# Performance work log

Measured on AMD Instinct MI355X. Metric: run time of the kernel, lower is better.

The kernel has to match this reference:

```python
import jax, jax.numpy as jnp
import numpy as np

N_TOKEN = 267735
CUTS = [0, 20000, 40000, 200000, 267735]
DIV = 4
D_MODEL = 1024
N_HEAD = 16
D_HEAD = 64
D_INNER = 4096
N_LAYER = 4
QLEN = 512
MLEN = 512
BSZ = 4
EPS = 1e-5


def _ln(x, g, b):
    mu = jnp.mean(x, axis=-1, keepdims=True)
    var = jnp.var(x, axis=-1, keepdims=True)
    return (x - mu) * jax.lax.rsqrt(var + EPS) * g + b


def _rel_shift(x):
    # x: [qlen, klen, bsz, n_head]
    q, k, b, n = x.shape
    x = jnp.pad(x, ((0, 0), (1, 0), (0, 0), (0, 0)))
    x = x.reshape(k + 1, q, b, n)[1:]
    return x.reshape(q, k, b, n)


def setup_inputs() -> dict:
    key = jax.random.key(0)
    ks = list(jax.random.split(key, 32))
    p = lambda i, shape: 0.02 * jax.random.normal(ks[i], shape, dtype=jnp.float32)
    inp = {}
    inp['input_ids'] = jax.random.randint(ks[0], (BSZ, QLEN), 0, N_TOKEN, dtype=jnp.int32)
    inp['mems'] = 0.05 * jax.random.normal(ks[1], (N_LAYER, MLEN, BSZ, D_MODEL), dtype=jnp.float32)
    # adaptive embedding: cluster tables + projections (div_val=4)
    for i in range(4):
        l, r = CUTS[i], CUTS[i + 1]
        d_i = D_MODEL // (DIV ** i)
        inp[f'emb{i}'] = p(2 + i, (r - l, d_i))
        inp[f'proj{i}'] = p(6 + i, (d_i, D_MODEL))
    H = N_HEAD * D_HEAD
    inp['qkv_W'] = p(10, (N_LAYER, D_MODEL, 3 * H))
    inp['r_W'] = p(11, (N_LAYER, D_MODEL, H))
    inp['o_W'] = p(12, (N_LAYER, H, D_MODEL))
    inp['r_w_bias'] = p(13, (N_LAYER, N_HEAD, D_HEAD))
    inp['r_r_bias'] = p(14, (N_LAYER, N_HEAD, D_HEAD))
    inp['ln1_g'] = jnp.ones((N_LAYER, D_MODEL), jnp.float32)
    inp['ln1_b'] = jnp.zeros((N_LAYER, D_MODEL), jnp.float32)
    inp['ff_w1'] = p(15, (N_LAYER, D_MODEL, D_INNER))
    inp['ff_b1'] = jnp.zeros((N_LAYER, D_INNER), jnp.float32)
    inp['ff_w2'] = p(16, (N_LAYER, D_INNER, D_MODEL))
    inp['ff_b2'] = jnp.zeros((N_LAYER, D_MODEL), jnp.float32)
    inp['ln2_g'] = jnp.ones((N_LAYER, D_MODEL), jnp.float32)
    inp['ln2_b'] = jnp.zeros((N_LAYER, D_MODEL), jnp.float32)
    return inp


def _forward(input_ids, mems, embs, projs, qkv_W, r_W, o_W, r_w_bias, r_r_bias,
             ln1_g, ln1_b, ff_w1, ff_b1, ff_w2, ff_b2, ln2_g, ln2_b):
    ids = input_ids.T  # [qlen, bsz]
    qlen, bsz = ids.shape
    mems = jax.lax.stop_gradient(mems)  # mems are detached in the original
    mlen = mems.shape[1]
    klen = qlen + mlen

    # --- adaptive embedding (masked gather + scatter-add, same math as boolean_mask/scatter_nd) ---
    flat = ids.reshape(-1)
    emb = jnp.zeros((flat.shape[0], D_MODEL), jnp.float32)
    for i in range(4):
        l, r = CUTS[i], CUTS[i + 1]
        mask = (flat >= l) & (flat < r)
        idx = jnp.clip(flat - l, 0, r - l - 1)
        e_i = jnp.einsum('id,de->ie', embs[i][idx], projs[i])
        emb = emb + jnp.where(mask[:, None], e_i, 0.0)
    word_emb = (emb * (D_MODEL ** 0.5)).reshape(qlen, bsz, D_MODEL)

    # --- sinusoidal relative positions, pos_seq = klen-1 .. 0 ---
    pos_seq = jnp.arange(klen - 1, -1, -1, dtype=jnp.float32)
    inv_freq = 1.0 / (10000.0 ** (jnp.arange(0, D_MODEL, 2, dtype=jnp.float32) / D_MODEL))
    sinusoid = jnp.einsum('i,j->ij', pos_seq, inv_freq)
    pos_emb = jnp.concatenate([jnp.sin(sinusoid), jnp.cos(sinusoid)], axis=-1)  # [klen, d_model]

    # causal mask over memory-extended keys: [qlen, klen]
    attn_mask = jnp.triu(jnp.ones((qlen, klen), jnp.float32), k=1 + mlen)
    mask4 = attn_mask[:, :, None, None]
    scale = 1.0 / (D_HEAD ** 0.5)

    h = word_emb
    for l in range(N_LAYER):
        cat = jnp.concatenate([mems[l], h], axis=0)  # [klen, bsz, d_model]
        w_heads = jnp.einsum('kbd,dh->kbh', cat, qkv_W[l])
        r_head_k = jnp.einsum('kd,dh->kh', pos_emb, r_W[l]).reshape(klen, N_HEAD, D_HEAD)
        q_h, k_h, v_h = jnp.split(w_heads, 3, axis=-1)
        q_h = q_h[-qlen:].reshape(qlen, bsz, N_HEAD, D_HEAD)
        k_h = k_h.reshape(klen, bsz, N_HEAD, D_HEAD)
        v_h = v_h.reshape(klen, bsz, N_HEAD, D_HEAD)
        AC = jnp.einsum('ibnd,jbnd->ijbn', q_h + r_w_bias[l], k_h)
        BD = _rel_shift(jnp.einsum('ibnd,jnd->ijbn', q_h + r_r_bias[l], r_head_k))
        score = (AC + BD) * scale
        score = score * (1.0 - mask4) - 1e30 * mask4
        prob = jax.nn.softmax(score, axis=1)
        attn_vec = jnp.einsum('ijbn,jbnd->ibnd', prob, v_h).reshape(qlen, bsz, N_HEAD * D_HEAD)
        attn_out = jnp.einsum('ibh,hd->ibd', attn_vec, o_W[l])
        h = _ln(h + attn_out, ln1_g[l], ln1_b[l])
        ff = jnp.einsum('ibf,fd->ibd', jax.nn.relu(jnp.einsum('ibd,df->ibf', h, ff_w1[l]) + ff_b1[l]), ff_w2[l]) + ff_b2[l]
        h = _ln(h + ff, ln2_g[l], ln2_b[l])

    return h.transpose(1, 0, 2)  # [bsz, qlen, d_model]


def reference(input_ids, mems, emb0, emb1, emb2, emb3, proj0, proj1, proj2, proj3,
              qkv_W, r_W, o_W, r_w_bias, r_r_bias, ln1_g, ln1_b,
              ff_w1, ff_b1, ff_w2, ff_b2, ln2_g, ln2_b):
    return _forward(input_ids, mems, (emb0, emb1, emb2, emb3), (proj0, proj1, proj2, proj3),
                    qkv_W, r_W, o_W, r_w_bias, r_r_bias, ln1_g, ln1_b,
                    ff_w1, ff_b1, ff_w2, ff_b2, ln2_g, ln2_b)
```

## Files before the change

### kernel.cpp

```cpp
#include <hip/hip_runtime.h>

typedef __attribute__((ext_vector_type(8))) short bf16x8;
typedef __attribute__((ext_vector_type(4))) float f32x4;

#define N_LAYER 4
#define QLEN 512
#define MLEN 512
#define KLEN 1024
#define BSZ 4
#define DM 1024
#define NH 16
#define DH 64
#define DINNER 4096
#define EK 1408
#define BDLD 1152

__device__ __forceinline__ unsigned short f2bf(float x) {
    unsigned u = __float_as_uint(x);
    u += 0x7fffu + ((u >> 16) & 1u);
    return (unsigned short)(u >> 16);
}
__device__ __forceinline__ float bf2f(unsigned short v) {
    return __uint_as_float(((unsigned)v) << 16);
}

__device__ __forceinline__ void gload16(const unsigned short* g, unsigned short* l) {
    __builtin_amdgcn_global_load_lds(
        (const __attribute__((address_space(1))) unsigned int*)g,
        (__attribute__((address_space(3))) unsigned int*)l, 16, 0, 0);
}

__device__ __forceinline__ bf16x8 lds_read8_sw(const unsigned short* base, int row, int cb) {
    return *(const bf16x8*)((const char*)base + row * 128 + (cb ^ ((row & 7) << 4)));
}

__global__ __launch_bounds__(256)
void transpose_all(const float* __restrict__ qkvWl, const float* __restrict__ rWl,
                   const float* __restrict__ oWl, const float* __restrict__ w1l,
                   const float* __restrict__ w2l,
                   unsigned short* __restrict__ qkvT, unsigned short* __restrict__ rT,
                   unsigned short* __restrict__ oT, unsigned short* __restrict__ w1T,
                   unsigned short* __restrict__ w2T) {
    __shared__ float tile[64][65];
    int id = blockIdx.x;
    const float* W; unsigned short* D; int K, N, bx, by;
    if (id < 768)       { W = qkvWl; D = qkvT; K = 1024; N = 3072; bx = id % 48; by = id / 48; }
    else if (id < 1024) { id -= 768;  W = rWl;  D = rT;  K = 1024; N = 1024; bx = id & 15; by = id >> 4; }
    else if (id < 1280) { id -= 1024; W = oWl;  D = oT;  K = 1024; N = 1024; bx = id & 15; by = id >> 4; }
    else if (id < 2304) { id -= 1280; W = w1l;  D = w1T; K = 1024; N = 4096; bx = id & 63; by = id >> 6; }
    else                { id -= 2304; W = w2l;  D = w2T; K = 4096; N = 1024; bx = id & 15; by = id >> 4; }
    const int tid = threadIdx.x;
#pragma unroll
    for (int s = 0; s < 4; ++s) {
        int idx = s * 256 + tid;
        int kr = idx >> 4, c4 = (idx & 15) * 4;
        float4 v = *(const float4*)(W + (size_t)(by * 64 + kr) * N + bx * 64 + c4);
        tile[kr][c4] = v.x; tile[kr][c4 + 1] = v.y;
        tile[kr][c4 + 2] = v.z; tile[kr][c4 + 3] = v.w;
    }
    __syncthreads();
#pragma unroll
    for (int s = 0; s < 2; ++s) {
        int idx = s * 256 + tid;
        int nl = idx >> 3, k8 = (idx & 7) * 8;
        unsigned short tmp[8];
#pragma unroll
        for (int j = 0; j < 8; ++j) tmp[j] = f2bf(tile[k8 + j][nl]);
        *(uint4*)(D + (size_t)(bx * 64 + nl) * K + by * 64 + k8) = *(uint4*)tmp;
    }
}

__global__ __launch_bounds__(256)
void transpose_pad(const float* __restrict__ W, unsigned short* __restrict__ dst,
                   int K, int N, int dstLD, int dstOff) {
    __shared__ float tile[32][33];
    const int tx = threadIdx.x & 31, ty = threadIdx.x >> 5;
    const int bx = blockIdx.x, by = blockIdx.y;
#pragma unroll
    for (int i = 0; i < 4; ++i) {
        int k = by * 32 + ty + i * 8;
        tile[ty + i * 8][tx] = (k < K) ? W[(size_t)k * N + bx * 32 + tx] : 0.f;
    }
    __syncthreads();
#pragma unroll
    for (int i = 0; i < 4; ++i) {
        int n = bx * 32 + ty + i * 8;
        int k = by * 32 + tx;
        dst[(size_t)n * dstLD + dstOff + k] = f2bf(tile[tx][ty + i * 8]);
    }
}

__global__ __launch_bounds__(256)
void emb_gather(const int* __restrict__ ids,
                const float* __restrict__ e0, const float* __restrict__ e1,
                const float* __restrict__ e2, const float* __restrict__ e3,
                unsigned short* __restrict__ embA) {
    const int chunk = blockIdx.x * 256 + threadIdx.x;
    if (chunk >= 2048 * 176) return;
    const int t = chunk / 176;
    const int e8 = (chunk - t * 176) * 8;
    const int i = t >> 2, b = t & 3;
    const int id = ids[b * QLEN + i];
    const float* src = nullptr;
    if (e8 < 1024) {
        if (id < 20000) src = e0 + (size_t)id * 1024 + e8;
    } else if (e8 < 1280) {
        if (id >= 20000 && id < 40000) src = e1 + (size_t)(id - 20000) * 256 + (e8 - 1024);
    } else if (e8 < 1344) {
        if (id >= 40000 && id < 200000) src = e2 + (size_t)(id - 40000) * 64 + (e8 - 1280);
    } else if (e8 < 1360) {
        if (id >= 200000) src = e3 + (size_t)(id - 200000) * 16 + (e8 - 1344);
    }
    uint4 o = {0u, 0u, 0u, 0u};
    if (src) {
        float4 v0 = *(const float4*)src;
        float4 v1 = *(const float4*)(src + 4);
        o.x = (unsigned)f2bf(v0.x * 32.f) | ((unsigned)f2bf(v0.y * 32.f) << 16);
        o.y = (unsigned)f2bf(v0.z * 32.f) | ((unsigned)f2bf(v0.w * 32.f) << 16);
        o.z = (unsigned)f2bf(v1.x * 32.f) | ((unsigned)f2bf(v1.y * 32.f) << 16);
        o.w = (unsigned)f2bf(v1.z * 32.f) | ((unsigned)f2bf(v1.w * 32.f) << 16);
    }
    *(uint4*)(embA + (size_t)t * EK + e8) = o;
}

template <int MODE, int BN>
__global__ __launch_bounds__(256)
void gemm_bt(const unsigned short* __restrict__ A, const unsigned short* __restrict__ BT,
             float* __restrict__ C, unsigned short* __restrict__ Cbf,
             const float* __restrict__ bias,
             const float* __restrict__ rwb, const float* __restrict__ rrb,
             unsigned short* __restrict__ Qw, unsigned short* __restrict__ Qr,
             unsigned short* __restrict__ Kb, unsigned short* __restrict__ VTb,
             int M, int N, int K) {
    constexpr int NF = BN / 32;
    __shared__ unsigned short lA[2][128 * 64];
    __shared__ unsigned short lB[2][BN * 64];
    const int tid = threadIdx.x;
    const int w = tid >> 6, l = tid & 63;
    const int lane15 = l & 15, lh = l >> 4;
    const int nwg = gridDim.x;
    const int cpx = nwg >> 3;
    const int swz = (blockIdx.x & 7) * cpx + (blockIdx.x >> 3);
    const int nbn = N / BN;
    const int bm = swz / nbn, bn = swz % nbn;
    const int wr = (w >> 1) * 64, wc = (w & 1) * (BN / 2);

    f32x4 acc[4][NF] = {};

    const unsigned short* gA = A + (size_t)(bm * 128) * K;
    const unsigned short* gB = BT + (size_t)(bn * BN) * K;

    auto stage = [&](int buf, int k0) {
#pragma unroll
        for (int s = 0; s < 4; ++s) {
            int g = tid + s * 256, row = g >> 3;
            gload16(gA + (size_t)row * K + k0 + ((g & 7) ^ (row & 7)) * 8,
                    lA[buf] + g * 8);
        }
#pragma unroll
        for (int s = 0; s < BN / 32; ++s) {
            int g = tid + s * 256, row = g >> 3;
            gload16(gB + (size_t)row * K + k0 + ((g & 7) ^ (row & 7)) * 8,
                    lB[buf] + g * 8);
        }
    };

    stage(0, 0);
    __syncthreads();
    int cur = 0;
    for (int k0 = 0; k0 < K; k0 += 64) {
        if (k0 + 64 < K) stage(cur ^ 1, k0 + 64);
        const unsigned short* cA = lA[cur];
        const unsigned short* cB = lB[cur];
#pragma unroll
        for (int kk = 0; kk < 2; ++kk) {
            bf16x8 af[4], bfr[NF];
#pragma unroll
            for (int f = 0; f < 4; ++f)
                af[f] = lds_read8_sw(cA, wr + f * 16 + lane15, kk * 64 + lh * 16);
#pragma unroll
            for (int f = 0; f < NF; ++f)
                bfr[f] = lds_read8_sw(cB, wc + f * 16 + lane15, kk * 64 + lh * 16);
#pragma unroll
            for (int mi = 0; mi < 4; ++mi)
#pragma unroll
                for (int ni = 0; ni < NF; ++ni)
                    acc[mi][ni] = __builtin_amdgcn_mfma_f32_16x16x32_bf16(
                        af[mi], bfr[ni], acc[mi][ni], 0, 0, 0);
        }
        __syncthreads();
        cur ^= 1;
    }

#pragma unroll
    for (int mi = 0; mi < 4; ++mi) {
        int rowb = bm * 128 + wr + mi * 16 + lh * 4;
#pragma unroll
        for (int ni = 0; ni < NF; ++ni) {
            int col = bn * BN + wc + ni * 16 + lane15;
#pragma unroll
            for (int r = 0; r < 4; ++r) {
                float x = acc[mi][ni][r];
                if (MODE == 0) {
                    C[(size_t)(rowb + r) * N + col] = x;
                } else if (MODE == 1) {
                    x += bias[col];
                    Cbf[(size_t)(rowb + r) * N + col] = f2bf(x > 0.f ? x : 0.f);
                } else if (MODE == 2) {
                    C[(size_t)(rowb + r) * N + col] = x + bias[col];
                } else if (MODE == 3) {
                    int j = rowb >> 2;
                    int bb_ = r;
                    if (col < 1024) {
                        if (j >= MLEN) {
                            int i = j - MLEN, n = col >> 6, d = col & 63;
                            size_t o = ((size_t)(bb_ * NH + n) * QLEN + i) * DH + d;
                            Qw[o] = f2bf((x + rwb[col]) * 0.125f);
                            Qr[o] = f2bf(x + rrb[col]);
                        }
                    } else if (col < 2048) {
                        int c2 = col - 1024, n = c2 >> 6, d = c2 & 63;
                        Kb[((size_t)(bb_ * NH + n) * KLEN + j) * DH + d] = f2bf(x);
                    } else {
                        int c2 = col - 2048, n = c2 >> 6, d = c2 & 63;
                        VTb[((size_t)(bb_ * NH + n) * DH + d) * KLEN + j] = f2bf(x);
                    }
                } else {
                    int j = rowb + r;
                    int n = col >> 6, d = col & 63;
                    Kb[((size_t)n * KLEN + j) * DH + d] = f2bf(x);
                }
            }
        }
    }
}

__global__ __launch_bounds__(256)
void bd_gemm(const unsigned short* __restrict__ Qr, const unsigned short* __restrict__ Rb,
             unsigned short* __restrict__ BDs) {
    __shared__ unsigned short lA[128 * 64];
    __shared__ unsigned short lB[128 * 64];
    const int tid = threadIdx.x;
    const int w = tid >> 6, l = tid & 63;
    const int lane15 = l & 15, lh = l >> 4;
    const int blk = blockIdx.x;
    const int bn = blk & 63;
    const int tile = blk >> 6;
    const int mi_ = tile & 3, nj = tile >> 2;
    const int n = bn & 15;
    const int wr = (w >> 1) * 64, wc = (w & 1) * 64;

    const unsigned short* gA = Qr + (size_t)bn * QLEN * DH + (size_t)(mi_ * 128) * 64;
    const unsigned short* gB = Rb + (size_t)n * KLEN * DH + (size_t)(nj * 128) * 64;
#pragma unroll
    for (int s = 0; s < 4; ++s) {
        int g = tid + s * 256, row = g >> 3;
        gload16(gA + (size_t)row * 64 + ((g & 7) ^ (row & 7)) * 8, lA + g * 8);
        gload16(gB + (size_t)row * 64 + ((g & 7) ^ (row & 7)) * 8, lB + g * 8);
    }
    __syncthreads();
    f32x4 acc[4][4] = {};
#pragma unroll
    for (int kk = 0; kk < 2; ++kk) {
        bf16x8 af[4], bfr[4];
#pragma unroll
        for (int f = 0; f < 4; ++f) {
            af[f]  = lds_read8_sw(lA, wr + f * 16 + lane15, kk * 64 + lh * 16);
            bfr[f] = lds_read8_sw(lB, wc + f * 16 + lane15, kk * 64 + lh * 16);
        }
#pragma unroll
        for (int mi = 0; mi < 4; ++mi)
#pragma unroll
            for (int ni = 0; ni < 4; ++ni)
                acc[mi][ni] = __builtin_amdgcn_mfma_f32_16x16x32_bf16(
                    af[mi], bfr[ni], acc[mi][ni], 0, 0, 0);
    }
    unsigned short* out = BDs + (size_t)bn * 512 * BDLD;
#pragma unroll
    for (int mi = 0; mi < 4; ++mi) {
        int rowb = mi_ * 128 + wr + mi * 16 + lh * 4;
#pragma unroll
        for (int ni = 0; ni < 4; ++ni) {
            int col = nj * 128 + wc + ni * 16 + lane15;
#pragma unroll
            for (int r = 0; r < 4; ++r)
                out[(size_t)(rowb + r) * BDLD + col] = f2bf(acc[mi][ni][r] * 0.125f);
        }
    }
}

__global__ __launch_bounds__(256)
void pos_kernel(unsigned short* __restrict__ posbf) {
    const int p = blockIdx.x, tid = threadIdx.x;
    const float ps = (float)(KLEN - 1 - p);
    const float c = -2.0f * 9.210340371976184f / 1024.0f;
#pragma unroll
    for (int j4 = 0; j4 < 4; ++j4) {
        int j = tid + j4 * 256;
        int m = (j < 512) ? j : j - 512;
        float freq = __expf((float)m * c);
        float ang = ps * freq;
        float v = (j < 512) ? sinf(ang) : cosf(ang);
        posbf[(size_t)p * DM + j] = f2bf(v);
    }
}

__global__ __launch_bounds__(256)
void cat_kernel(const float* __restrict__ mem_l, const float* __restrict__ h,
                unsigned short* __restrict__ catbf) {
    const int t = blockIdx.x, tid = threadIdx.x;
    const float* src = (t < 2048) ? (mem_l + (size_t)t * DM) : (h + (size_t)(t - 2048) * DM);
    float4 v = ((const float4*)src)[tid];
    uint2 o;
    o.x = (unsigned)f2bf(v.x) | ((unsigned)f2bf(v.y) << 16);
    o.y = (unsigned)f2bf(v.z) | ((unsigned)f2bf(v.w) << 16);
    ((uint2*)(catbf + (size_t)t * DM))[tid] = o;
}

__global__ __launch_bounds__(64)
void attn_part(const unsigned short* __restrict__ Qw,
               const unsigned short* __restrict__ Kb, const unsigned short* __restrict__ VTb,
               const unsigned short* __restrict__ BDs,
               unsigned short* __restrict__ Opart, float* __restrict__ ms) {
    __shared__ unsigned short lP[16 * 64];

    const int l = threadIdx.x;
    const int lane15 = l & 15, lh = l >> 4;
    const int blk = blockIdx.x;
    const int bn = blk & 63;
    const int rest = blk >> 6;
    const int rg = rest & 3;
    const int c = rest >> 2;

    const int offt[8] = {0, 3, 7, 11, 15, 20, 25, 30};
    const int nctt[8] = {3, 4, 4, 4, 5, 5, 5, 6};
    int it = 0;
#pragma unroll
    for (int i = 1; i < 8; ++i) if (c >= offt[i]) it = i;
    const int cl = c - offt[it];
    const int nck = nctt[it];
    const int ntiles = it + 9;
    const int jt0 = (cl * ntiles) / nck;
    const int jt1 = ((cl + 1) * ntiles) / nck;
    const int i0 = it * 64;
    const int rowl = rg * 16 + lh * 4;

    bf16x8 qw[2];
    {
        size_t qb = ((size_t)bn * QLEN + i0 + rg * 16 + lane15) * DH + lh * 8;
        qw[0] = *(const bf16x8*)(Qw + qb);
        qw[1] = *(const bf16x8*)(Qw + qb + 32);
    }
    bf16x8 onesb;
#pragma unroll
    for (int j = 0; j < 8; ++j) onesb[j] = (short)0x3F80;

    const unsigned short* kp = Kb + (size_t)bn * KLEN * DH + (size_t)(jt0 * 64 + lane15) * DH + lh * 8;
    const unsigned short* vp = VTb + (size_t)bn * DH * KLEN + (size_t)lane15 * KLEN + jt0 * 64 + lh * 8;
    const unsigned short* bdp[4];
#pragma unroll
    for (int r = 0; r < 4; ++r) {
        int row = i0 + rowl + r;
        bdp[r] = BDs + (size_t)bn * 512 * BDLD + (size_t)row * BDLD
                 + (511 - row) + jt0 * 64 + lane15;
    }

    f32x4 oacc[4] = {};
    f32x4 srowv = {};

    for (int jt = jt0; jt < jt1; ++jt) {
        float bdv[4][4];
#pragma unroll
        for (int f = 0; f < 4; ++f)
#pragma unroll
            for (int r = 0; r < 4; ++r)
                bdv[f][r] = bf2f(bdp[r][16 * f]);

        bf16x8 kf[2][4];
#pragma unroll
        for (int f = 0; f < 4; ++f) {
            const unsigned short* p = kp + (size_t)(f * 16) * DH;
            kf[0][f] = *(const bf16x8*)p;
            kf[1][f] = *(const bf16x8*)(p + 32);
        }

        f32x4 sac[4] = {};
        __builtin_amdgcn_s_setprio(1);
#pragma unroll
        for (int kk = 0; kk < 2; ++kk)
#pragma unroll
            for (int f = 0; f < 4; ++f)
                sac[f] = __builtin_amdgcn_mfma_f32_16x16x32_bf16(qw[kk], kf[kk][f], sac[f], 0, 0, 0);
        __builtin_amdgcn_s_setprio(0);

        bf16x8 vf[2][4];
#pragma unroll
        for (int kk = 0; kk < 2; ++kk)
#pragma unroll
            for (int f = 0; f < 4; ++f)
                vf[kk][f] = *(const bf16x8*)(vp + (size_t)(f * 16) * KLEN + kk * 32);

        const bool lastTile = (jt == it + 8);
        float pv[4][4];
#pragma unroll
        for (int f = 0; f < 4; ++f) {
            int lj = lane15 + 16 * f;
#pragma unroll
            for (int r = 0; r < 4; ++r) {
                float s = sac[f][r] + bdv[f][r];
                if (lastTile && (lj > rowl + r)) s = -1e30f;
                pv[f][r] = __expf(s - 8.f);
            }
        }

#pragma unroll
        for (int f = 0; f < 4; ++f)
#pragma unroll
            for (int r = 0; r < 4; ++r) {
                int row = lh * 4 + r, cb2 = (lane15 + 16 * f) * 2;
                *(unsigned short*)((char*)lP + row * 128 + (cb2 ^ ((row & 7) << 4))) =
                    f2bf(pv[f][r]);
            }
        bf16x8 pa[2];
        pa[0] = lds_read8_sw(lP, lane15, lh * 16);
        pa[1] = lds_read8_sw(lP, lane15, 64 + lh * 16);

        __builtin_amdgcn_s_setprio(1);
#pragma unroll
        for (int kk = 0; kk < 2; ++kk) {
#pragma unroll
            for (int f = 0; f < 4; ++f)
                oacc[f] = __builtin_amdgcn_mfma_f32_16x16x32_bf16(pa[kk], vf[kk][f], oacc[f], 0, 0, 0);
            srowv = __builtin_amdgcn_mfma_f32_16x16x32_bf16(pa[kk], onesb, srowv, 0, 0, 0);
        }
        __builtin_amdgcn_s_setprio(0);

        kp += 64 * DH;
        vp += 64;
#pragma unroll
        for (int r = 0; r < 4; ++r) bdp[r] += 64;
    }

    const int slot = (bn * 8 + it) * 6 + cl;
    unsigned short* Op = Opart + (size_t)slot * 4096;
#pragma unroll
    for (int f = 0; f < 4; ++f)
#pragma unroll
        for (int r = 0; r < 4; ++r)
            Op[(rowl + r) * 64 + lane15 + 16 * f] = f2bf(oacc[f][r]);
    if (lane15 == 0) {
        float* msp = ms + (size_t)slot * 64;
#pragma unroll
        for (int r = 0; r < 4; ++r) msp[rowl + r] = srowv[r];
    }
}

__global__ __launch_bounds__(256)
void attn_merge(const unsigned short* __restrict__ Opart, const float* __restrict__ ms,
                unsigned short* __restrict__ avec) {
    const int blk = blockIdx.x;
    const int bn = blk & 63, it = blk >> 6;
    const int n = bn & 15, b = bn >> 4;
    const int nctt[8] = {3, 4, 4, 4, 5, 5, 5, 6};
    const int k = nctt[it];
    const int tid = threadIdx.x;
    const int r = tid >> 2, cq = (tid & 3) * 16;
    const int base_slot = (bn * 8 + it) * 6;

    float S = 0.f;
    for (int c = 0; c < k; ++c) S += ms[(size_t)(base_slot + c) * 64 + r];

    float acc[16];
#pragma unroll
    for (int j = 0; j < 16; ++j) acc[j] = 0.f;
    for (int c = 0; c < k; ++c) {
        const bf16x8* op = (const bf16x8*)(Opart + (size_t)(base_slot + c) * 4096 + r * 64 + cq);
        bf16x8 v0 = op[0], v1 = op[1];
#pragma unroll
        for (int j = 0; j < 8; ++j) {
            acc[j]     += bf2f((unsigned short)v0[j]);
            acc[8 + j] += bf2f((unsigned short)v1[j]);
        }
    }
    float inv = 1.0f / S;
    int t = (it * 64 + r) * 4 + b;
    unsigned short* dst = avec + (size_t)t * DM + n * 64 + cq;
#pragma unroll
    for (int j = 0; j < 16; ++j) dst[j] = f2bf(acc[j] * inv);
}

__global__ __launch_bounds__(256)
void ln_kernel(const float* __restrict__ hin, const float* __restrict__ res,
               const float* __restrict__ g, const float* __restrict__ bb,
               float* __restrict__ hout, unsigned short* __restrict__ hbf) {
    __shared__ float ls[8];
    const int t = blockIdx.x, tid = threadIdx.x;
    float4 x = ((const float4*)(hin + (size_t)t * DM))[tid];
    float4 rr = ((const float4*)(res + (size_t)t * DM))[tid];
    float v0 = x.x + rr.x, v1 = x.y + rr.y, v2 = x.z + rr.z, v3 = x.w + rr.w;
    float s = v0 + v1 + v2 + v3;
    float sq = v0 * v0 + v1 * v1 + v2 * v2 + v3 * v3;
#pragma unroll
    for (int off = 1; off < 64; off <<= 1) {
        s += __shfl_xor(s, off);
        sq += __shfl_xor(sq, off);
    }
    const int w = tid >> 6;
    if ((tid & 63) == 0) { ls[w] = s; ls[4 + w] = sq; }
    __syncthreads();
    s = ls[0] + ls[1] + ls[2] + ls[3];
    sq = ls[4] + ls[5] + ls[6] + ls[7];
    float mu = s * (1.f / 1024.f);
    float var = sq * (1.f / 1024.f) - mu * mu;
    float rstd = rsqrtf(var + 1e-5f);
    float y[4] = {v0, v1, v2, v3};
    float4 of;
    uint2 ob;
    float* op = &of.x;
#pragma unroll
    for (int j = 0; j < 4; ++j) {
        int d = tid * 4 + j;
        op[j] = (y[j] - mu) * rstd * g[d] + bb[d];
    }
    ob.x = (unsigned)f2bf(of.x) | ((unsigned)f2bf(of.y) << 16);
    ob.y = (unsigned)f2bf(of.z) | ((unsigned)f2bf(of.w) << 16);
    ((float4*)(hout + (size_t)t * DM))[tid] = of;
    ((uint2*)(hbf + (size_t)t * DM))[tid] = ob;
}

__global__ __launch_bounds__(256)
void out_kernel(const float* __restrict__ h, float* __restrict__ out) {
    const int t = blockIdx.x, tid = threadIdx.x;
    const int i = t >> 2, b = t & 3;
    ((float4*)(out + ((size_t)b * QLEN + i) * DM))[tid] =
        ((const float4*)(h + (size_t)t * DM))[tid];
}

extern "C" void kernel_launch(void* const* d_in, const int* in_sizes, int n_in,
                              void* d_out, int out_size, void* d_ws, size_t ws_size,
                              hipStream_t stream) {
    const int* ids = (const int*)d_in[0];
    const float* mems = (const float*)d_in[1];
    const float* embp[4] = {nullptr, nullptr, nullptr, nullptr};
    const float* projp[4] = {nullptr, nullptr, nullptr, nullptr};
    const long long esz[4] = {20000LL * 1024, 20000LL * 256, 160000LL * 64, 67735LL * 16};
    const long long psz[4] = {1024LL * 1024, 256LL * 1024, 64LL * 1024, 16LL * 1024};
    for (int idx = 2; idx <= 9 && idx < n_in; ++idx) {
        long long s = in_sizes[idx];
        for (int c = 0; c < 4; ++c) {
            if (s == esz[c]) embp[c] = (const float*)d_in[idx];
            else if (s == psz[c]) projp[c] = (const float*)d_in[idx];
        }
    }
    const float* qkvW = (const float*)d_in[10];
    const float* rW   = (const float*)d_in[11];
    const float* oW   = (const float*)d_in[12];
    const float* rwb  = (const float*)d_in[13];
    const float* rrb  = (const float*)d_in[14];
    const float* ln1g = (const float*)d_in[15];
    const float* ln1b = (const float*)d_in[16];
    const float* ffw1 = (const float*)d_in[17];
    const float* ffb1 = (const float*)d_in[18];
    const float* ffw2 = (const float*)d_in[19];
    const float* ffb2 = (const float*)d_in[20];
    const float* ln2g = (const float*)d_in[21];
    const float* ln2b = (const float*)d_in[22];

    size_t off = 0;
    char* base = (char*)d_ws;
    auto alloc = [&](size_t bytes) -> char* {
        char* p = base + off;
        off = (off + bytes + 255) & ~(size_t)255;
        return p;
    };
    unsigned short* qkvT  = (unsigned short*)alloc(3072ull * 1024 * 2);
    unsigned short* rT    = (unsigned short*)alloc(1024ull * 1024 * 2);
    unsigned short* oT    = (unsigned short*)alloc(1024ull * 1024 * 2);
    unsigned short* w1T   = (unsigned short*)alloc(4096ull * 1024 * 2);
    unsigned short* w2T   = (unsigned short*)alloc(1024ull * 4096 * 2);
    unsigned short* embA  = (unsigned short*)alloc(2048ull * EK * 2);
    unsigned short* embBT = (unsigned short*)alloc(1024ull * EK * 2);
    float* h              = (float*)alloc(2048ull * 1024 * 4);
    unsigned short* hbf   = (unsigned short*)alloc(2048ull * 1024 * 2);
    unsigned short* catb  = (unsigned short*)alloc(4096ull * 1024 * 2);
    unsigned short* posb  = (unsigned short*)alloc(1024ull * 1024 * 2);
    unsigned short* Qw    = (unsigned short*)alloc(4ull * 16 * 512 * 64 * 2);
    unsigned short* Qr    = (unsigned short*)alloc(4ull * 16 * 512 * 64 * 2);
    unsigned short* Kb    = (unsigned short*)alloc(4ull * 16 * 1024 * 64 * 2);
    unsigned short* VTb   = (unsigned short*)alloc(4ull * 16 * 1024 * 64 * 2);
    unsigned short* Rb    = (unsigned short*)alloc(16ull * 1024 * 64 * 2);
    unsigned short* avec  = (unsigned short*)alloc(2048ull * 1024 * 2);
    float* resid          = (float*)alloc(2048ull * 1024 * 4);
    unsigned short* ff1b  = (unsigned short*)alloc(2048ull * 4096 * 2);
    unsigned short* Opart = (unsigned short*)alloc(3072ull * 4096 * 2);
    float* msbuf          = (float*)alloc(3072ull * 64 * 4);
    unsigned short* BDs   = (unsigned short*)alloc(64ull * 512 * BDLD * 2);
    (void)ws_size; (void)out_size;

    emb_gather<<<(2048 * 176 + 255) / 256, 256, 0, stream>>>(
        ids, embp[0], embp[1], embp[2], embp[3], embA);
    transpose_pad<<<dim3(32, 32), 256, 0, stream>>>(projp[0], embBT, 1024, 1024, EK, 0);
    transpose_pad<<<dim3(32, 8),  256, 0, stream>>>(projp[1], embBT, 256,  1024, EK, 1024);
    transpose_pad<<<dim3(32, 2),  256, 0, stream>>>(projp[2], embBT, 64,   1024, EK, 1280);
    transpose_pad<<<dim3(32, 2),  256, 0, stream>>>(projp[3], embBT, 16,   1024, EK, 1344);
    pos_kernel<<<1024, 256, 0, stream>>>(posb);
    gemm_bt<0, 128><<<(2048 / 128) * (1024 / 128), 256, 0, stream>>>(
        embA, embBT, h, nullptr, nullptr, nullptr, nullptr, nullptr, nullptr, nullptr, nullptr,
        2048, 1024, EK);

    for (int l = 0; l < N_LAYER; ++l) {
        const float* qkvWl = qkvW + (size_t)l * 1024 * 3072;
        const float* rWl   = rW + (size_t)l * 1024 * 1024;
        const float* oWl   = oW + (size_t)l * 1024 * 1024;
        const float* w1l   = ffw1 + (size_t)l * 1024 * 4096;
        const float* w2l   = ffw2 + (size_t)l * 4096 * 1024;

        transpose_all<<<3328, 256, 0, stream>>>(qkvWl, rWl, oWl, w1l, w2l,
                                                qkvT, rT, oT, w1T, w2T);

        cat_kernel<<<4096, 256, 0, stream>>>(mems + (size_t)l * 2048 * 1024, h, catb);

        gemm_bt<3, 128><<<(4096 / 128) * (3072 / 128), 256, 0, stream>>>(
            catb, qkvT, nullptr, nullptr, nullptr,
            rwb + l * 1024, rrb + l * 1024, Qw, Qr, Kb, VTb, 4096, 3072, 1024);

        gemm_bt<4, 64><<<(1024 / 128) * (1024 / 64), 256, 0, stream>>>(
            posb, rT, nullptr, nullptr, nullptr,
            nullptr, nullptr, nullptr, nullptr, Rb, nullptr, 1024, 1024, 1024);

        bd_gemm<<<64 * 32, 256, 0, stream>>>(Qr, Rb, BDs);

        attn_part<<<64 * 144, 64, 0, stream>>>(Qw, Kb, VTb, BDs, Opart, msbuf);
        attn_merge<<<512, 256, 0, stream>>>(Opart, msbuf, avec);

        gemm_bt<0, 64><<<(2048 / 128) * (1024 / 64), 256, 0, stream>>>(
            avec, oT, resid, nullptr, nullptr, nullptr, nullptr, nullptr, nullptr, nullptr, nullptr,
            2048, 1024, 1024);
        ln_kernel<<<2048, 256, 0, stream>>>(h, resid, ln1g + l * 1024, ln1b + l * 1024, h, hbf);

        gemm_bt<1, 128><<<(2048 / 128) * (4096 / 128), 256, 0, stream>>>(
            hbf, w1T, nullptr, ff1b, ffb1 + l * 4096, nullptr, nullptr, nullptr, nullptr, nullptr, nullptr,
            2048, 4096, 1024);
        gemm_bt<2, 64><<<(2048 / 128) * (1024 / 64), 256, 0, stream>>>(
            ff1b, w2T, resid, nullptr, ffb2 + l * 1024, nullptr, nullptr, nullptr, nullptr, nullptr, nullptr,
            2048, 1024, 4096);
        ln_kernel<<<2048, 256, 0, stream>>>(h, resid, ln2g + l * 1024, ln2b + l * 1024, h, hbf);
    }

    out_kernel<<<2048, 256, 0, stream>>>(h, (float*)d_out);
}
```

Measured before the change: 1.128 ms.

## Prefetch K/V tiles in attention and write h bf16 directly into concat buffer

```diff
diff --git a/kernel.cpp b/kernel.cpp
--- a/kernel.cpp
+++ b/kernel.cpp
@@ -225,10 +225,13 @@
                         int c2 = col - 2048, n = c2 >> 6, d = c2 & 63;
                         VTb[((size_t)(bb_ * NH + n) * DH + d) * KLEN + j] = f2bf(x);
                     }
-                } else {
+                } else if (MODE == 4) {
                     int j = rowb + r;
                     int n = col >> 6, d = col & 63;
                     Kb[((size_t)n * KLEN + j) * DH + d] = f2bf(x);
+                } else {
+                    C[(size_t)(rowb + r) * N + col] = x;
+                    Cbf[(size_t)(rowb + r) * N + col] = f2bf(x);
                 }
             }
         }
@@ -306,11 +309,9 @@
 }
 
 __global__ __launch_bounds__(256)
-void cat_kernel(const float* __restrict__ mem_l, const float* __restrict__ h,
-                unsigned short* __restrict__ catbf) {
+void mems_cat(const float* __restrict__ mem_l, unsigned short* __restrict__ catbf) {
     const int t = blockIdx.x, tid = threadIdx.x;
-    const float* src = (t < 2048) ? (mem_l + (size_t)t * DM) : (h + (size_t)(t - 2048) * DM);
-    float4 v = ((const float4*)src)[tid];
+    float4 v = ((const float4*)(mem_l + (size_t)t * DM))[tid];
     uint2 o;
     o.x = (unsigned)f2bf(v.x) | ((unsigned)f2bf(v.y) << 16);
     o.y = (unsigned)f2bf(v.z) | ((unsigned)f2bf(v.w) << 16);
@@ -342,6 +343,7 @@
     const int ntiles = it + 9;
     const int jt0 = (cl * ntiles) / nck;
     const int jt1 = ((cl + 1) * ntiles) / nck;
+    const int nt = jt1 - jt0;
     const int i0 = it * 64;
     const int rowl = rg * 16 + lh * 4;
 
@@ -368,21 +370,28 @@
     f32x4 oacc[4] = {};
     f32x4 srowv = {};
 
-    for (int jt = jt0; jt < jt1; ++jt) {
-        float bdv[4][4];
-#pragma unroll
-        for (int f = 0; f < 4; ++f)
-#pragma unroll
-            for (int r = 0; r < 4; ++r)
-                bdv[f][r] = bf2f(bdp[r][16 * f]);
-
-        bf16x8 kf[2][4];
+    auto loadt = [&](bf16x8 (&kf)[2][4], bf16x8 (&vf)[2][4], int d) {
 #pragma unroll
         for (int f = 0; f < 4; ++f) {
-            const unsigned short* p = kp + (size_t)(f * 16) * DH;
+            const unsigned short* p = kp + (size_t)(d * 64 + f * 16) * DH;
             kf[0][f] = *(const bf16x8*)p;
             kf[1][f] = *(const bf16x8*)(p + 32);
         }
+#pragma unroll
+        for (int kk = 0; kk < 2; ++kk)
+#pragma unroll
+            for (int f = 0; f < 4; ++f)
+                vf[kk][f] = *(const bf16x8*)(vp + d * 64 + (size_t)(f * 16) * KLEN + kk * 32);
+    };
+
+    auto computet = [&](bf16x8 (&kf)[2][4], bf16x8 (&vf)[2][4], int jt) {
+        const int d = jt - jt0;
+        float bdv[4][4];
+#pragma unroll
+        for (int f = 0; f < 4; ++f)
+#pragma unroll
+            for (int r = 0; r < 4; ++r)
+                bdv[f][r] = bf2f(bdp[r][d * 64 + 16 * f]);
 
         f32x4 sac[4] = {};
         __builtin_amdgcn_s_setprio(1);
@@ -392,13 +401,6 @@
             for (int f = 0; f < 4; ++f)
                 sac[f] = __builtin_amdgcn_mfma_f32_16x16x32_bf16(qw[kk], kf[kk][f], sac[f], 0, 0, 0);
         __builtin_amdgcn_s_setprio(0);
-
-        bf16x8 vf[2][4];
-#pragma unroll
-        for (int kk = 0; kk < 2; ++kk)
-#pragma unroll
-            for (int f = 0; f < 4; ++f)
-                vf[kk][f] = *(const bf16x8*)(vp + (size_t)(f * 16) * KLEN + kk * 32);
 
         const bool lastTile = (jt == it + 8);
         float pv[4][4];
@@ -412,7 +414,6 @@
                 pv[f][r] = __expf(s - 8.f);
             }
         }
-
 #pragma unroll
         for (int f = 0; f < 4; ++f)
 #pragma unroll
@@ -421,24 +422,31 @@
                 *(unsigned short*)((char*)lP + row * 128 + (cb2 ^ ((row & 7) << 4))) =
                     f2bf(pv[f][r]);
             }
-        bf16x8 pa[2];
-        pa[0] = lds_read8_sw(lP, lane15, lh * 16);
-        pa[1] = lds_read8_sw(lP, lane15, 64 + lh * 16);
+        bf16x8 pa0 = lds_read8_sw(lP, lane15, lh * 16);
+        bf16x8 pa1 = lds_read8_sw(lP, lane15, 64 + lh * 16);
 
         __builtin_amdgcn_s_setprio(1);
 #pragma unroll
-        for (int kk = 0; kk < 2; ++kk) {
-#pragma unroll
-            for (int f = 0; f < 4; ++f)
-                oacc[f] = __builtin_amdgcn_mfma_f32_16x16x32_bf16(pa[kk], vf[kk][f], oacc[f], 0, 0, 0);
-            srowv = __builtin_amdgcn_mfma_f32_16x16x32_bf16(pa[kk], onesb, srowv, 0, 0, 0);
-        }
+        for (int f = 0; f < 4; ++f)
+            oacc[f] = __builtin_amdgcn_mfma_f32_16x16x32_bf16(pa0, vf[0][f], oacc[f], 0, 0, 0);
+        srowv = __builtin_amdgcn_mfma_f32_16x16x32_bf16(pa0, onesb, srowv, 0, 0, 0);
+#pragma unroll
+        for (int f = 0; f < 4; ++f)
+            oacc[f] = __builtin_amdgcn_mfma_f32_16x16x32_bf16(pa1, vf[1][f], oacc[f], 0, 0, 0);
+        srowv = __builtin_amdgcn_mfma_f32_16x16x32_bf16(pa1, onesb, srowv, 0, 0, 0);
         __builtin_amdgcn_s_setprio(0);
-
-        kp += 64 * DH;
-        vp += 64;
-#pragma unroll
-        for (int r = 0; r < 4; ++r) bdp[r] += 64;
+    };
+
+    bf16x8 kfA[2][4], vfA[2][4], kfB[2][4], vfB[2][4];
+    loadt(kfA, vfA, 0);
+    if (nt >= 2) loadt(kfB, vfB, 1);
+    computet(kfA, vfA, jt0);
+    if (nt == 2) {
+        computet(kfB, vfB, jt0 + 1);
+    } else if (nt >= 3) {
+        loadt(kfA, vfA, 2);
+        computet(kfB, vfB, jt0 + 1);
+        computet(kfA, vfA, jt0 + 2);
     }
 
     const int slot = (bn * 8 + it) * 6 + cl;
@@ -597,6 +605,8 @@
     unsigned short* BDs   = (unsigned short*)alloc(64ull * 512 * BDLD * 2);
     (void)ws_size; (void)out_size;
 
+    unsigned short* catbHi = catb + 2048ull * 1024;
+
     emb_gather<<<(2048 * 176 + 255) / 256, 256, 0, stream>>>(
         ids, embp[0], embp[1], embp[2], embp[3], embA);
     transpose_pad<<<dim3(32, 32), 256, 0, stream>>>(projp[0], embBT, 1024, 1024, EK, 0);
@@ -604,8 +614,8 @@
     transpose_pad<<<dim3(32, 2),  256, 0, stream>>>(projp[2], embBT, 64,   1024, EK, 1280);
     transpose_pad<<<dim3(32, 2),  256, 0, stream>>>(projp[3], embBT, 16,   1024, EK, 1344);
     pos_kernel<<<1024, 256, 0, stream>>>(posb);
-    gemm_bt<0, 128><<<(2048 / 128) * (1024 / 128), 256, 0, stream>>>(
-        embA, embBT, h, nullptr, nullptr, nullptr, nullptr, nullptr, nullptr, nullptr, nullptr,
+    gemm_bt<5, 128><<<(2048 / 128) * (1024 / 128), 256, 0, stream>>>(
+        embA, embBT, h, catbHi, nullptr, nullptr, nullptr, nullptr, nullptr, nullptr, nullptr,
         2048, 1024, EK);
 
     for (int l = 0; l < N_LAYER; ++l) {
@@ -618,7 +628,7 @@
         transpose_all<<<3328, 256, 0, stream>>>(qkvWl, rWl, oWl, w1l, w2l,
                                                 qkvT, rT, oT, w1T, w2T);
 
-        cat_kernel<<<4096, 256, 0, stream>>>(mems + (size_t)l * 2048 * 1024, h, catb);
+        mems_cat<<<2048, 256, 0, stream>>>(mems + (size_t)l * 2048 * 1024, catb);
 
         gemm_bt<3, 128><<<(4096 / 128) * (3072 / 128), 256, 0, stream>>>(
             catb, qkvT, nullptr, nullptr, nullptr,
@@ -644,7 +654,8 @@
         gemm_bt<2, 64><<<(2048 / 128) * (1024 / 64), 256, 0, stream>>>(
             ff1b, w2T, resid, nullptr, ffb2 + l * 1024, nullptr, nullptr, nullptr, nullptr, nullptr, nullptr,
             2048, 1024, 4096);
-        ln_kernel<<<2048, 256, 0, stream>>>(h, resid, ln2g + l * 1024, ln2b + l * 1024, h, hbf);
+        ln_kernel<<<2048, 256, 0, stream>>>(h, resid, ln2g + l * 1024, ln2b + l * 1024, h,
+                                            (l < 3) ? catbHi : hbf);
     }
 
     out_kernel<<<2048, 256, 0, stream>>>(h, (float*)d_out);
```

Measured after the change: 1.142 ms. Within noise of the previous version (+1.2%).

## Skip query projection on memory rows, fuse R projection into QKV GEMM, trim BD tiles

Applied to the files above, without the earlier changes.

```diff
diff --git a/kernel.cpp b/kernel.cpp
--- a/kernel.cpp
+++ b/kernel.cpp
@@ -127,11 +127,7 @@
 __global__ __launch_bounds__(256)
 void gemm_bt(const unsigned short* __restrict__ A, const unsigned short* __restrict__ BT,
              float* __restrict__ C, unsigned short* __restrict__ Cbf,
-             const float* __restrict__ bias,
-             const float* __restrict__ rwb, const float* __restrict__ rrb,
-             unsigned short* __restrict__ Qw, unsigned short* __restrict__ Qr,
-             unsigned short* __restrict__ Kb, unsigned short* __restrict__ VTb,
-             int M, int N, int K) {
+             const float* __restrict__ bias, int M, int N, int K) {
     constexpr int NF = BN / 32;
     __shared__ unsigned short lA[2][128 * 64];
     __shared__ unsigned short lB[2][BN * 64];
@@ -208,27 +204,107 @@
                     Cbf[(size_t)(rowb + r) * N + col] = f2bf(x > 0.f ? x : 0.f);
                 } else if (MODE == 2) {
                     C[(size_t)(rowb + r) * N + col] = x + bias[col];
-                } else if (MODE == 3) {
-                    int j = rowb >> 2;
-                    int bb_ = r;
+                } else {
+                    C[(size_t)(rowb + r) * N + col] = x;
+                    Cbf[(size_t)(rowb + r) * N + col] = f2bf(x);
+                }
+            }
+        }
+    }
+}
+
+__global__ __launch_bounds__(256)
+void qkv_rk_gemm(const unsigned short* __restrict__ catb, const unsigned short* __restrict__ posb,
+                 const unsigned short* __restrict__ qkvT, const unsigned short* __restrict__ rT,
+                 const float* __restrict__ rwb, const float* __restrict__ rrb,
+                 unsigned short* __restrict__ Qw, unsigned short* __restrict__ Qr,
+                 unsigned short* __restrict__ Kb, unsigned short* __restrict__ VTb,
+                 unsigned short* __restrict__ Rb) {
+    __shared__ unsigned short lA[2][128 * 64];
+    __shared__ unsigned short lB[2][128 * 64];
+    const int tid = threadIdx.x;
+    const int w = tid >> 6, l = tid & 63;
+    const int lane15 = l & 15, lh = l >> 4;
+    const int cpx = gridDim.x >> 3;
+    const int swz = (blockIdx.x & 7) * cpx + (blockIdx.x >> 3);
+    const int wr = (w >> 1) * 64, wc = (w & 1) * 64;
+
+    const unsigned short* gA;
+    const unsigned short* gB;
+    int part, bm, bn;
+    if (swz < 512)      { part = 0; bm = swz >> 4; bn = swz & 15;
+                          gA = catb + (size_t)(bm * 128) * 1024;
+                          gB = qkvT + (size_t)(1024 + bn * 128) * 1024; }
+    else if (swz < 640) { part = 1; int q = swz - 512; bm = q >> 3; bn = q & 7;
+                          gA = catb + (size_t)(2048 + bm * 128) * 1024;
+                          gB = qkvT + (size_t)(bn * 128) * 1024; }
+    else                { part = 2; int q = swz - 640; bm = q >> 3; bn = q & 7;
+                          gA = posb + (size_t)(bm * 128) * 1024;
+                          gB = rT + (size_t)(bn * 128) * 1024; }
+
+    f32x4 acc[4][4] = {};
+    auto stage = [&](int buf, int k0) {
+#pragma unroll
+        for (int s = 0; s < 4; ++s) {
+            int g = tid + s * 256, row = g >> 3;
+            gload16(gA + (size_t)row * 1024 + k0 + ((g & 7) ^ (row & 7)) * 8, lA[buf] + g * 8);
+            gload16(gB + (size_t)row * 1024 + k0 + ((g & 7) ^ (row & 7)) * 8, lB[buf] + g * 8);
+        }
+    };
+    stage(0, 0);
+    __syncthreads();
+    int cur = 0;
+    for (int k0 = 0; k0 < 1024; k0 += 64) {
+        if (k0 + 64 < 1024) stage(cur ^ 1, k0 + 64);
+        const unsigned short* cA = lA[cur];
+        const unsigned short* cB = lB[cur];
+#pragma unroll
+        for (int kk = 0; kk < 2; ++kk) {
+            bf16x8 af[4], bfr[4];
+#pragma unroll
+            for (int f = 0; f < 4; ++f) {
+                af[f]  = lds_read8_sw(cA, wr + f * 16 + lane15, kk * 64 + lh * 16);
+                bfr[f] = lds_read8_sw(cB, wc + f * 16 + lane15, kk * 64 + lh * 16);
+            }
+#pragma unroll
+            for (int mi = 0; mi < 4; ++mi)
+#pragma unroll
+                for (int ni = 0; ni < 4; ++ni)
+                    acc[mi][ni] = __builtin_amdgcn_mfma_f32_16x16x32_bf16(
+                        af[mi], bfr[ni], acc[mi][ni], 0, 0, 0);
+        }
+        __syncthreads();
+        cur ^= 1;
+    }
+
+#pragma unroll
+    for (int mi = 0; mi < 4; ++mi) {
+        int rowb = bm * 128 + wr + mi * 16 + lh * 4;
+#pragma unroll
+        for (int ni = 0; ni < 4; ++ni) {
+            int col = bn * 128 + wc + ni * 16 + lane15;
+#pragma unroll
+            for (int r = 0; r < 4; ++r) {
+                float x = acc[mi][ni][r];
+                if (part == 0) {
+                    int j = rowb >> 2, bb_ = r;
                     if (col < 1024) {
-                        if (j >= MLEN) {
-                            int i = j - MLEN, n = col >> 6, d = col & 63;
-                            size_t o = ((size_t)(bb_ * NH + n) * QLEN + i) * DH + d;
-                            Qw[o] = f2bf((x + rwb[col]) * 0.125f);
-                            Qr[o] = f2bf(x + rrb[col]);
-                        }
-                    } else if (col < 2048) {
-                        int c2 = col - 1024, n = c2 >> 6, d = c2 & 63;
+                        int n = col >> 6, d = col & 63;
                         Kb[((size_t)(bb_ * NH + n) * KLEN + j) * DH + d] = f2bf(x);
                     } else {
-                        int c2 = col - 2048, n = c2 >> 6, d = c2 & 63;
+                        int c2 = col - 1024, n = c2 >> 6, d = c2 & 63;
                         VTb[((size_t)(bb_ * NH + n) * DH + d) * KLEN + j] = f2bf(x);
                     }
+                } else if (part == 1) {
+                    int i = rowb >> 2, bb_ = r;
+                    int n = col >> 6, d = col & 63;
+                    size_t o = ((size_t)(bb_ * NH + n) * QLEN + i) * DH + d;
+                    Qw[o] = f2bf((x + rwb[col]) * 0.125f);
+                    Qr[o] = f2bf(x + rrb[col]);
                 } else {
                     int j = rowb + r;
                     int n = col >> 6, d = col & 63;
-                    Kb[((size_t)n * KLEN + j) * DH + d] = f2bf(x);
+                    Rb[((size_t)n * KLEN + j) * DH + d] = f2bf(x);
                 }
             }
         }
@@ -246,7 +322,9 @@
     const int blk = blockIdx.x;
     const int bn = blk & 63;
     const int tile = blk >> 6;
-    const int mi_ = tile & 3, nj = tile >> 2;
+    const int bd_mi[26] = {0,0,0,0,0, 1,1,1,1,1,1, 2,2,2,2,2,2,2, 3,3,3,3,3,3,3,3};
+    const int bd_nj[26] = {3,4,5,6,7, 2,3,4,5,6,7, 1,2,3,4,5,6,7, 0,1,2,3,4,5,6,7};
+    const int mi_ = bd_mi[tile], nj = bd_nj[tile];
     const int n = bn & 15;
     const int wr = (w >> 1) * 64, wc = (w & 1) * 64;
 
@@ -306,11 +384,9 @@
 }
 
 __global__ __launch_bounds__(256)
-void cat_kernel(const float* __restrict__ mem_l, const float* __restrict__ h,
-                unsigned short* __restrict__ catbf) {
+void mems_cat(const float* __restrict__ mem_l, unsigned short* __restrict__ catbf) {
     const int t = blockIdx.x, tid = threadIdx.x;
-    const float* src = (t < 2048) ? (mem_l + (size_t)t * DM) : (h + (size_t)(t - 2048) * DM);
-    float4 v = ((const float4*)src)[tid];
+    float4 v = ((const float4*)(mem_l + (size_t)t * DM))[tid];
     uint2 o;
     o.x = (unsigned)f2bf(v.x) | ((unsigned)f2bf(v.y) << 16);
     o.y = (unsigned)f2bf(v.z) | ((unsigned)f2bf(v.w) << 16);
@@ -597,6 +673,8 @@
     unsigned short* BDs   = (unsigned short*)alloc(64ull * 512 * BDLD * 2);
     (void)ws_size; (void)out_size;
 
+    unsigned short* catbHi = catb + 2048ull * 1024;
+
     emb_gather<<<(2048 * 176 + 255) / 256, 256, 0, stream>>>(
         ids, embp[0], embp[1], embp[2], embp[3], embA);
     transpose_pad<<<dim3(32, 32), 256, 0, stream>>>(projp[0], embBT, 1024, 1024, EK, 0);
@@ -604,9 +682,8 @@
     transpose_pad<<<dim3(32, 2),  256, 0, stream>>>(projp[2], embBT, 64,   1024, EK, 1280);
     transpose_pad<<<dim3(32, 2),  256, 0, stream>>>(projp[3], embBT, 16,   1024, EK, 1344);
     pos_kernel<<<1024, 256, 0, stream>>>(posb);
-    gemm_bt<0, 128><<<(2048 / 128) * (1024 / 128), 256, 0, stream>>>(
-        embA, embBT, h, nullptr, nullptr, nullptr, nullptr, nullptr, nullptr, nullptr, nullptr,
-        2048, 1024, EK);
+    gemm_bt<5, 128><<<(2048 / 128) * (1024 / 128), 256, 0, stream>>>(
+        embA, embBT, h, catbHi, nullptr, 2048, 1024, EK);
 
     for (int l = 0; l < N_LAYER; ++l) {
         const float* qkvWl = qkvW + (size_t)l * 1024 * 3072;
@@ -618,33 +695,27 @@
         transpose_all<<<3328, 256, 0, stream>>>(qkvWl, rWl, oWl, w1l, w2l,
                                                 qkvT, rT, oT, w1T, w2T);
 
-        cat_kernel<<<4096, 256, 0, stream>>>(mems + (size_t)l * 2048 * 1024, h, catb);
-
-        gemm_bt<3, 128><<<(4096 / 128) * (3072 / 128), 256, 0, stream>>>(
-            catb, qkvT, nullptr, nullptr, nullptr,
-            rwb + l * 1024, rrb + l * 1024, Qw, Qr, Kb, VTb, 4096, 3072, 1024);
-
-        gemm_bt<4, 64><<<(1024 / 128) * (1024 / 64), 256, 0, stream>>>(
-            posb, rT, nullptr, nullptr, nullptr,
-            nullptr, nullptr, nullptr, nullptr, Rb, nullptr, 1024, 1024, 1024);
-
-        bd_gemm<<<64 * 32, 256, 0, stream>>>(Qr, Rb, BDs);
+        mems_cat<<<2048, 256, 0, stream>>>(mems + (size_t)l * 2048 * 1024, catb);
+
+        qkv_rk_gemm<<<704, 256, 0, stream>>>(catb, posb, qkvT, rT,
+                                             rwb + l * 1024, rrb + l * 1024,
+                                             Qw, Qr, Kb, VTb, Rb);
+
+        bd_gemm<<<64 * 26, 256, 0, stream>>>(Qr, Rb, BDs);
 
         attn_part<<<64 * 144, 64, 0, stream>>>(Qw, Kb, VTb, BDs, Opart, msbuf);
         attn_merge<<<512, 256, 0, stream>>>(Opart, msbuf, avec);
 
         gemm_bt<0, 64><<<(2048 / 128) * (1024 / 64), 256, 0, stream>>>(
-            avec, oT, resid, nullptr, nullptr, nullptr, nullptr, nullptr, nullptr, nullptr, nullptr,
-            2048, 1024, 1024);
+            avec, oT, resid, nullptr, nullptr, 2048, 1024, 1024);
         ln_kernel<<<2048, 256, 0, stream>>>(h, resid, ln1g + l * 1024, ln1b + l * 1024, h, hbf);
 
         gemm_bt<1, 128><<<(2048 / 128) * (4096 / 128), 256, 0, stream>>>(
-            hbf, w1T, nullptr, ff1b, ffb1 + l * 4096, nullptr, nullptr, nullptr, nullptr, nullptr, nullptr,
-            2048, 4096, 1024);
+            hbf, w1T, nullptr, ff1b, ffb1 + l * 4096, 2048, 4096, 1024);
         gemm_bt<2, 64><<<(2048 / 128) * (1024 / 64), 256, 0, stream>>>(
-            ff1b, w2T, resid, nullptr, ffb2 + l * 1024, nullptr, nullptr, nullptr, nullptr, nullptr, nullptr,
-            2048, 1024, 4096);
-        ln_kernel<<<2048, 256, 0, stream>>>(h, resid, ln2g + l * 1024, ln2b + l * 1024, h, hbf);
+            ff1b, w2T, resid, nullptr, ffb2 + l * 1024, 2048, 1024, 4096);
+        ln_kernel<<<2048, 256, 0, stream>>>(h, resid, ln2g + l * 1024, ln2b + l * 1024, h,
+                                            (l < 3) ? catbHi : hbf);
     }
 
     out_kernel<<<2048, 256, 0, stream>>>(h, (float*)d_out);
```

New measurement: 1.078 ms. 1.05x faster.
